# Kernel tuning notes

Measured on AMD Instinct MI355X. Metric: run time of the kernel, lower is better.

Reference implementation:

```python
import jax, jax.numpy as jnp
import numpy as np
from jax import lax

DIM = 384
HEADS = 8
CROP = 8


def conv2d(x, w, groups=1, pad=0):
    return lax.conv_general_dilated(
        x, w, (1, 1), ((pad, pad), (pad, pad)),
        dimension_numbers=("NCHW", "OIHW", "NCHW"),
        feature_group_count=groups)


def l2norm(x, axis):
    # F.normalize: x / max(||x||_2, 1e-12)
    n = jnp.sqrt(jnp.sum(x * x, axis=axis, keepdims=True))
    return x / jnp.maximum(n, 1e-12)


def masked_softmax(a, k):
    # top-k mask via k-th largest threshold (equivalent to scatter mask for
    # continuous-valued scores), then softmax with -inf fill.
    kth = lax.top_k(a, k)[0][..., -1:]
    return jax.nn.softmax(jnp.where(a >= kth, a, -jnp.inf), axis=-1)


def setup_inputs() -> dict:
    key = jax.random.key(0)
    ks = jax.random.split(key, 5)
    b, c, h, w = 2, DIM, 128, 128
    x = jax.random.normal(ks[0], (b, c, h, w), dtype=jnp.float32)
    w_qkv = jax.random.normal(ks[1], (3 * c, c, 1, 1), dtype=jnp.float32) * 0.02
    w_dw = jax.random.normal(ks[2], (3 * c, 1, 3, 3), dtype=jnp.float32) * 0.02
    w_proj = jax.random.normal(ks[3], (c, c, 1, 1), dtype=jnp.float32) * 0.02
    temperature = jnp.ones((HEADS, 1, 1), dtype=jnp.float32)
    a = jnp.full((1,), 0.2, dtype=jnp.float32)
    return {"x": x, "w_qkv": w_qkv, "w_dw": w_dw, "w_proj": w_proj,
            "temperature": temperature, "attn1": a, "attn2": a,
            "attn3": a, "attn4": a}


def reference(x, w_qkv, w_dw, w_proj, temperature, attn1, attn2, attn3, attn4):
    b, c, h, w = x.shape
    heads, crop = HEADS, CROP
    ch = c // heads                      # per-head channels C
    N = crop * crop                      # window tokens

    qkv = conv2d(conv2d(x, w_qkv), w_dw, groups=3 * c, pad=1)
    q, k, v = jnp.split(qkv, 3, axis=1)

    def to_heads(t):                     # b (head c) h w -> b head c (h w)
        return t.reshape(b, heads, ch, h * w)

    def to_win(t):                       # imgtowindows on (b, head, c, h, w)
        t = t.reshape(b, heads, ch, h // crop, crop, w // crop, crop)
        t = jnp.transpose(t, (0, 1, 3, 5, 4, 6, 2))
        return t.reshape(-1, heads, N, ch)

    qc, kc, vc = to_heads(q), to_heads(k), to_heads(v)
    qs = to_win(q.reshape(b, heads, ch, h, w))
    ks_ = to_win(k.reshape(b, heads, ch, h, w))
    vs = to_win(v.reshape(b, heads, ch, h, w))

    qc, kc = l2norm(qc, -1), l2norm(kc, -1)
    qs, ks_ = l2norm(qs, -1), l2norm(ks_, -1)

    cattn = jnp.einsum("bhcn,bhdn->bhcd", qc, kc) * temperature  # (b,H,C,C)
    sattn = jnp.einsum("bhnc,bhmc->bhnm", qs, ks_) * temperature  # (B',H,N,N)

    cks = [ch // 2, (ch * 2) // 3, (ch * 3) // 4, (ch * 4) // 5]
    sks = [N // 2, (N * 2) // 3, (N * 3) // 4, (N * 4) // 5]
    wts = [attn1, attn2, attn3, attn4]

    cout = sum((masked_softmax(cattn, kk) @ vc) * wt for kk, wt in zip(cks, wts))
    sout = sum((masked_softmax(sattn, kk) @ vs) * wt for kk, wt in zip(sks, wts))

    # windowstoimg (replicates torch's contiguous view/reshape semantics)
    sout = sout.reshape(b, heads, h, w, ch)
    sout = jnp.transpose(sout, (0, 1, 4, 2, 3)).reshape(b, heads, ch, h * w)

    out = (sout + cout).reshape(b, c, h, w)
    return conv2d(out, w_proj)
```

## Files before the change

kernel.cpp:

```cpp
#include <hip/hip_runtime.h>
#include <hip/hip_bf16.h>


#define HW 16384
#define CDIM 384
#define NHEADS 8
#define CH 48
#define NCHUNK 128

typedef __hip_bfloat16 bf16;
typedef __attribute__((ext_vector_type(8))) short short8;
typedef __attribute__((ext_vector_type(4))) float f32x4;

static __device__ __forceinline__ unsigned short f2bf_bits(float v) {
  bf16 b = __float2bfloat16(v);
  return __builtin_bit_cast(unsigned short, b);
}
static __device__ __forceinline__ float bfbits2f(unsigned short u) {
  return __bfloat162float(__builtin_bit_cast(bf16, u));
}

template <int CTRL>
static __device__ __forceinline__ float dppf(float x) {
  return __builtin_bit_cast(
      float, __builtin_amdgcn_update_dpp(0, __builtin_bit_cast(int, x), CTRL,
                                         0xF, 0xF, true));
}

__global__ __launch_bounds__(256) void decomp_all(const float* __restrict__ wq,
                                                  const float* __restrict__ wp,
                                                  unsigned short* __restrict__ qh,
                                                  unsigned short* __restrict__ ql,
                                                  unsigned short* __restrict__ ph,
                                                  unsigned short* __restrict__ pl) {
  const int i = blockIdx.x * 256 + threadIdx.x;
  const int nq = 3 * CDIM * CDIM;
  if (i < nq) {
    const float v = wq[i];
    const unsigned short hb = f2bf_bits(v);
    qh[i] = hb;
    ql[i] = f2bf_bits(v - bfbits2f(hb));
  } else {
    const int k = i - nq;
    if (k < CDIM * CDIM) {
      const float v = wp[k];
      const unsigned short hb = f2bf_bits(v);
      ph[k] = hb;
      pl[k] = f2bf_bits(v - bfbits2f(hb));
    }
  }
}

__global__ __launch_bounds__(256) void transpose_frag(const float* __restrict__ src,
                                                      short8* __restrict__ dh,
                                                      short8* __restrict__ dl,
                                                      float* __restrict__ sumsq) {
  if (blockIdx.x == 0 && threadIdx.x < 192) {
    const float4 z = {0.f, 0.f, 0.f, 0.f};
    ((float4*)sumsq)[threadIdx.x] = z;
  }
  const int o = blockIdx.x * 256 + threadIdx.x;
  const int ptile = o / 768;
  const int rem = o - ptile * 768;
  const int kc = rem >> 6, lane = rem & 63;
  const int p = ptile * 16 + (lane & 15);
  const int kb = kc * 32 + (lane >> 4) * 8;
  short8 hh, ll;
#pragma unroll
  for (int j = 0; j < 8; j++) {
    float v = src[(size_t)(kb + j) * HW + p];
    unsigned short hb = f2bf_bits(v);
    hh[j] = (short)hb;
    ll[j] = (short)f2bf_bits(v - bfbits2f(hb));
  }
  dh[o] = hh;
  dl[o] = ll;
}

__global__ __launch_bounds__(256, 4) void gemm_mfma(const unsigned short* __restrict__ Wh,
                                                    const unsigned short* __restrict__ Wl,
                                                    const short8* __restrict__ Xh,
                                                    const short8* __restrict__ Xl,
                                                    float* __restrict__ Out) {
  const int tid = threadIdx.x;
  const int wave = tid >> 6, lane = tid & 63;
  const int lm = lane & 15, lq = lane >> 4;
  const int g = blockIdx.y * 128 + blockIdx.x;
  const int xcd = g & 7, i = g >> 3;
  const int bx = xcd * 16 + (i & 15);
  const int by = i >> 4;
  const int p0 = bx * 128;
  const int oc0 = by * 64;
  const int pt0 = bx * 8 + wave * 2;
  f32x4 acc[4][2] = {};
#pragma unroll
  for (int kc = 0; kc < 12; kc++) {
    short8 ah[4], al[4], bh[2], bl[2];
#pragma unroll
    for (int mt = 0; mt < 4; mt++) {
      const size_t off = (size_t)(oc0 + mt * 16 + lm) * 384 + kc * 32 + lq * 8;
      ah[mt] = *reinterpret_cast<const short8*>(Wh + off);
      al[mt] = *reinterpret_cast<const short8*>(Wl + off);
    }
#pragma unroll
    for (int nt = 0; nt < 2; nt++) {
      const size_t idx = (size_t)((pt0 + nt) * 12 + kc) * 64 + lane;
      bh[nt] = Xh[idx];
      bl[nt] = Xl[idx];
    }
#pragma unroll
    for (int mt = 0; mt < 4; mt++)
#pragma unroll
      for (int nt = 0; nt < 2; nt++) {
        acc[mt][nt] = __builtin_amdgcn_mfma_f32_16x16x32_bf16(ah[mt], bh[nt], acc[mt][nt], 0, 0, 0);
        acc[mt][nt] = __builtin_amdgcn_mfma_f32_16x16x32_bf16(ah[mt], bl[nt], acc[mt][nt], 0, 0, 0);
        acc[mt][nt] = __builtin_amdgcn_mfma_f32_16x16x32_bf16(al[mt], bh[nt], acc[mt][nt], 0, 0, 0);
      }
  }
#pragma unroll
  for (int mt = 0; mt < 4; mt++)
#pragma unroll
    for (int nt = 0; nt < 2; nt++)
#pragma unroll
      for (int r = 0; r < 4; r++) {
        const int oc = oc0 + mt * 16 + lq * 4 + r;
        const int p = p0 + (wave * 2 + nt) * 16 + lm;
        Out[(size_t)oc * HW + p] = acc[mt][nt][r];
      }
}

__global__ __launch_bounds__(256) void dwconv3(const float* __restrict__ A,
                                               const float* __restrict__ wdw,
                                               float* __restrict__ Bq) {
  const int e = blockIdx.x * 256 + threadIdx.x;
  const int x4 = e & 31;
  const int y = (e >> 5) & 127;
  const int ch = e >> 12;
  const int x0 = x4 << 2;
  float w[9];
#pragma unroll
  for (int t = 0; t < 9; t++) w[t] = wdw[ch * 9 + t];
  const float* Ap = A + (size_t)ch * HW;
  float4 acc = {0.f, 0.f, 0.f, 0.f};
#pragma unroll
  for (int ky = 0; ky < 3; ky++) {
    const int yy = y + ky - 1;
    if (yy < 0 || yy > 127) continue;
    const float* row = Ap + yy * 128;
    const float4 c = *(const float4*)(row + x0);
    const float l = (x4 == 0) ? 0.f : row[x0 - 1];
    const float r = (x4 == 31) ? 0.f : row[x0 + 4];
    const float w0 = w[ky * 3], w1 = w[ky * 3 + 1], w2 = w[ky * 3 + 2];
    acc.x += w0 * l + w1 * c.x + w2 * c.y;
    acc.y += w0 * c.x + w1 * c.y + w2 * c.z;
    acc.z += w0 * c.y + w1 * c.z + w2 * c.w;
    acc.w += w0 * c.z + w1 * c.w + w2 * r;
  }
  *(float4*)(Bq + (size_t)e * 4) = acc;
}

__global__ __launch_bounds__(256, 3) void cattn_partial(const float* __restrict__ Bq,
                                                        float* __restrict__ part,
                                                        float* __restrict__ sumsq) {
  __shared__ __align__(16) float qs[48 * 132];
  __shared__ __align__(16) float ks2[48 * 132];
  const int tid = threadIdx.x;
  const int chunk = blockIdx.x, h = blockIdx.y;
  const int p0 = chunk * 128;
#pragma unroll
  for (int i = 0; i < 12; i++) {
    const int s4 = tid + i * 256;
    const int t = s4 >= 1536;
    const int r4 = s4 - t * 1536;
    const int cc = r4 >> 5;
    const int px = (r4 & 31) << 2;
    const float4 v4 = *(const float4*)(Bq + (size_t)(t * CDIM + h * CH + cc) * HW + p0 + px);
    *(float4*)((t ? ks2 : qs) + cc * 132 + px) = v4;
  }
  __syncthreads();
  if (tid < 96) {
    const int t = tid >= 48;
    const int cc = t ? tid - 48 : tid;
    const float* src = (t ? ks2 : qs) + cc * 132;
    float s = 0.f;
#pragma unroll
    for (int p = 0; p < 128; p += 4) {
      const float4 v = *(const float4*)(src + p);
      s += v.x * v.x + v.y * v.y + v.z * v.z + v.w * v.w;
    }
    atomicAdd(&sumsq[t * CDIM + h * CH + cc], s);
  }
  const int tx = tid & 15, ty = tid >> 4;
  const float* qb = qs + (ty * 3) * 132;
  const float* kb = ks2 + (tx * 3) * 132;
  float acc[3][3] = {};
  for (int pl = 0; pl < 128; pl += 4) {
    float4 qv[3], kv[3];
#pragma unroll
    for (int ii = 0; ii < 3; ii++) qv[ii] = *(const float4*)(qb + ii * 132 + pl);
#pragma unroll
    for (int jj = 0; jj < 3; jj++) kv[jj] = *(const float4*)(kb + jj * 132 + pl);
#pragma unroll
    for (int ii = 0; ii < 3; ii++)
#pragma unroll
      for (int jj = 0; jj < 3; jj++)
        acc[ii][jj] += qv[ii].x * kv[jj].x + qv[ii].y * kv[jj].y +
                       qv[ii].z * kv[jj].z + qv[ii].w * kv[jj].w;
  }
  float* rp = part + (size_t)(h * NCHUNK + chunk) * 2304;
#pragma unroll
  for (int ii = 0; ii < 3; ii++)
#pragma unroll
    for (int jj = 0; jj < 3; jj++)
      rp[(ty * 3 + ii) * 48 + tx * 3 + jj] = acc[ii][jj];
}

__global__ __launch_bounds__(64) void chan_softmax(
    const float* __restrict__ part, const float* __restrict__ sumsq,
    const float* __restrict__ temp, const float* __restrict__ a1,
    const float* __restrict__ a2, const float* __restrict__ a3,
    const float* __restrict__ a4, float* __restrict__ W48) {
  const int blk = blockIdx.x;
  const int i = blk % 48;
  const int h = blk / 48;
  const int lane = threadIdx.x;
  const float t = temp[h];
  float a = -3.0e38f;
  if (lane < 48) {
    const float* pp = part + (size_t)h * NCHUNK * 2304 + i * 48 + lane;
    float r = 0.f;
#pragma unroll 8
    for (int c = 0; c < NCHUNK; c++) r += pp[(size_t)c * 2304];
    const float iq = 1.f / fmaxf(sqrtf(sumsq[h * CH + i]), 1e-12f);
    const float ik = 1.f / fmaxf(sqrtf(sumsq[CDIM + h * CH + lane]), 1e-12f);
    a = t * iq * ik * r;
  }
  float m = a;
  for (int o = 32; o; o >>= 1) m = fmaxf(m, __shfl_xor(m, o));
  float e = (lane < 48) ? expf(a - m) : 0.f;
  int gt = 0;
  for (int j = 0; j < 48; j++) {
    float vj = __shfl(a, j);
    gt += (vj > a) ? 1 : 0;
  }
  const int ksel[4] = {24, 32, 36, 38};
  const float wts[4] = {a1[0], a2[0], a3[0], a4[0]};
  float coef = 0.f;
#pragma unroll
  for (int kk = 0; kk < 4; kk++) {
    float sel = (gt < ksel[kk]) ? e : 0.f;
    for (int o = 32; o; o >>= 1) sel += __shfl_xor(sel, o);
    if (gt < ksel[kk]) coef += wts[kk] / sel;
  }
  if (lane < 48) W48[(size_t)blk * 48 + lane] = e * coef;
}

static __device__ __forceinline__ void conv_frag_k(int f, const float* kRaw,
                                                   short8* KFh, short8* KFl) {
  int nt, ks, slot;
  if (f < 256) { nt = f >> 6; ks = 0; slot = f & 63; }
  else { const int g2 = f - 256; nt = g2 >> 5; ks = 1; slot = g2 & 31; }
  const int tok = nt * 16 + (slot & 15);
  const int ch0 = ks * 32 + (slot >> 4) * 8;
  const float* src = kRaw + tok * 49 + ch0;
  short8 hh, ll;
#pragma unroll
  for (int j = 0; j < 8; j++) {
    const float v = src[j];
    const unsigned short hb = f2bf_bits(v);
    hh[j] = (short)hb;
    ll[j] = (short)f2bf_bits(v - bfbits2f(hb));
  }
  KFh[f] = hh;
  KFl[f] = ll;
}
static __device__ __forceinline__ int wfrag_off(int f) {
  int nt, n, k0;
  if (f < 192) { nt = f >> 6; const int slot = f & 63; n = slot & 15; k0 = (slot >> 4) * 8; }
  else { const int g2 = f - 192; nt = g2 >> 5; const int slot = g2 & 31; n = slot & 15; k0 = 32 + (slot >> 4) * 8; }
  return (nt * 16 + n) * 48 + k0;
}

__global__ __launch_bounds__(256, 4) void spatial_kernel(
    const float* __restrict__ Bq, const float* __restrict__ W48,
    const float* __restrict__ temp, const float* __restrict__ a1,
    const float* __restrict__ a2_, const float* __restrict__ a3,
    const float* __restrict__ a4, float* __restrict__ Cbuf) {
  __shared__ __align__(16) char smem[40192];
  float* qRaw = (float*)smem;
  float* kRaw = (float*)(smem + 12544);
  short8* KFh = (short8*)(smem + 25088);
  short8* KFl = (short8*)(smem + 31232);
  float* S_lds = (float*)smem;
  unsigned short* VTh = (unsigned short*)(smem + 16640);
  unsigned short* VTl = (unsigned short*)(smem + 23552);
  bf16* Pl = (bf16*)(smem + 30464);
  short8* WFh = (short8*)smem;
  short8* WFl = (short8*)(smem + 4608);
  float* O_lds = (float*)(smem + 16640);
  float* invQ = (float*)(smem + 39680);
  float* invK = (float*)(smem + 39936);

  const int bid = blockIdx.x;
  const int wid = ((bid & 7) << 8) | (bid >> 3);
  const int wx = wid & 15, wy = (wid >> 4) & 15;
  const int head = wid >> 8;
  const int tid = threadIdx.x;
  const int lane = tid & 63, w = tid >> 6;
  const int lm = lane & 15, lq = lane >> 4;
  const int ybase = wy * 8, xbase = wx * 8;
  const int y_out = wy * 8 + (wx >> 1);
  const int x0 = (wx & 1) * 64;
  const size_t hb = (size_t)(head * CH) * HW;
  const float* wsrc = W48 + (size_t)head * 2304;

#pragma unroll
  for (int i = 0; i < 6; i++) {
    const int s4 = tid + i * 256;
    const int t = s4 >= 768;
    const int r4 = s4 - t * 768;
    const int cc = r4 >> 4, nq = r4 & 15;
    const int n = nq * 4;
    const int y = ybase + (n >> 3), x = xbase + (n & 7);
    const float4 v4 = *(const float4*)(Bq + (size_t)(t * CDIM) * HW + hb +
                                       (size_t)cc * HW + y * 128 + x);
    float* dst = (t ? kRaw : qRaw) + n * 49 + cc;
    dst[0] = v4.x; dst[49] = v4.y; dst[98] = v4.z; dst[147] = v4.w;
  }
  float wpre0[8], wpre1[8];
  {
    const int off = wfrag_off(tid);
    const float4 a = *(const float4*)(wsrc + off);
    const float4 b = *(const float4*)(wsrc + off + 4);
    wpre0[0] = a.x; wpre0[1] = a.y; wpre0[2] = a.z; wpre0[3] = a.w;
    wpre0[4] = b.x; wpre0[5] = b.y; wpre0[6] = b.z; wpre0[7] = b.w;
  }
  if (tid < 32) {
    const int off = wfrag_off(256 + tid);
    const float4 a = *(const float4*)(wsrc + off);
    const float4 b = *(const float4*)(wsrc + off + 4);
    wpre1[0] = a.x; wpre1[1] = a.y; wpre1[2] = a.z; wpre1[3] = a.w;
    wpre1[4] = b.x; wpre1[5] = b.y; wpre1[6] = b.z; wpre1[7] = b.w;
  }
  __syncthreads();

  float4 vv[3];
#pragma unroll
  for (int i = 0; i < 3; i++) {
    const int e4 = tid + i * 256;
    const int cc = e4 >> 4, n = (e4 & 15) * 4;
    const int y = ybase + (n >> 3), x = xbase + (n & 7);
    vv[i] = *(const float4*)(Bq + (size_t)(2 * CDIM) * HW + hb +
                             (size_t)cc * HW + y * 128 + x);
  }
  float af[16];
  {
    const int px = y_out * 128 + x0 + (w * 16 + lm);
    const float* vpl = Bq + (size_t)(2 * CDIM) * HW + hb + px;
#pragma unroll
    for (int ks = 0; ks < 2; ks++)
#pragma unroll
      for (int j = 0; j < 8; j++) {
        const int ch = ks * 32 + lq * 8 + j;
        af[ks * 8 + j] = (ch < 48) ? vpl[(size_t)ch * HW] : 0.f;
      }
  }

  if (tid < 128) {
    const int t = tid >> 6, n = tid & 63;
    const float* src = (t ? kRaw : qRaw) + n * 49;
    float ssum = 0.f;
#pragma unroll
    for (int cc = 0; cc < 48; cc++) { float v = src[cc]; ssum += v * v; }
    const float iv = 1.f / fmaxf(sqrtf(ssum), 1e-12f);
    if (t) invK[n] = iv; else invQ[n] = iv * temp[head];
  }

  conv_frag_k(tid, kRaw, KFh, KFl);
  if (tid < 128) conv_frag_k(256 + tid, kRaw, KFh, KFl);

  short8 qh[2], ql[2];
#pragma unroll
  for (int ks = 0; ks < 2; ks++) {
    const int ch0 = ks * 32 + lq * 8;
    const float* qp = qRaw + (w * 16 + lm) * 49 + ch0;
#pragma unroll
    for (int j = 0; j < 8; j++) {
      const float v = (ch0 < 48) ? qp[j] : 0.f;
      const unsigned short hbts = f2bf_bits(v);
      qh[ks][j] = (short)hbts;
      ql[ks][j] = (short)f2bf_bits(v - bfbits2f(hbts));
    }
  }
  __syncthreads();

  f32x4 sacc[4] = {};
#pragma unroll
  for (int nt = 0; nt < 4; nt++) {
    const short8 kh0 = KFh[nt * 64 + lane];
    const short8 kl0 = KFl[nt * 64 + lane];
    sacc[nt] = __builtin_amdgcn_mfma_f32_16x16x32_bf16(qh[0], kh0, sacc[nt], 0, 0, 0);
    sacc[nt] = __builtin_amdgcn_mfma_f32_16x16x32_bf16(qh[0], kl0, sacc[nt], 0, 0, 0);
    sacc[nt] = __builtin_amdgcn_mfma_f32_16x16x32_bf16(ql[0], kh0, sacc[nt], 0, 0, 0);
    short8 kh1 = {0, 0, 0, 0, 0, 0, 0, 0}, kl1 = {0, 0, 0, 0, 0, 0, 0, 0};
    if (lane < 32) { kh1 = KFh[256 + nt * 32 + lane]; kl1 = KFl[256 + nt * 32 + lane]; }
    sacc[nt] = __builtin_amdgcn_mfma_f32_16x16x32_bf16(qh[1], kh1, sacc[nt], 0, 0, 0);
    sacc[nt] = __builtin_amdgcn_mfma_f32_16x16x32_bf16(qh[1], kl1, sacc[nt], 0, 0, 0);
    sacc[nt] = __builtin_amdgcn_mfma_f32_16x16x32_bf16(ql[1], kh1, sacc[nt], 0, 0, 0);
  }

  float iqv[4];
#pragma unroll
  for (int r = 0; r < 4; r++) iqv[r] = invQ[w * 16 + lq * 4 + r];
#pragma unroll
  for (int nt = 0; nt < 4; nt++) {
    const float ik = invK[nt * 16 + lm];
#pragma unroll
    for (int r = 0; r < 4; r++)
      S_lds[(w * 16 + lq * 4 + r) * 65 + nt * 16 + lm] = sacc[nt][r] * iqv[r] * ik;
  }
  __syncthreads();

#pragma unroll
  for (int i = 0; i < 3; i++) {
    const int e4 = tid + i * 256;
    const int cc = e4 >> 4, n = (e4 & 15) * 4;
    const float v0 = vv[i].x, v1 = vv[i].y, v2 = vv[i].z, v3 = vv[i].w;
    const unsigned short h0 = f2bf_bits(v0), h1 = f2bf_bits(v1),
                         h2 = f2bf_bits(v2), h3 = f2bf_bits(v3);
    const ushort4 hh = {h0, h1, h2, h3};
    const ushort4 ll = {f2bf_bits(v0 - bfbits2f(h0)), f2bf_bits(v1 - bfbits2f(h1)),
                        f2bf_bits(v2 - bfbits2f(h2)), f2bf_bits(v3 - bfbits2f(h3))};
    *(ushort4*)(VTh + cc * 72 + n) = hh;
    *(ushort4*)(VTl + cc * 72 + n) = ll;
  }

  const float wts[4] = {a1[0], a2_[0], a3[0], a4[0]};
  const int sidx[4] = {32, 22, 16, 13};
#pragma unroll 4
  for (int rr = 0; rr < 16; rr++) {
    const int row = w * 16 + rr;
    const float a = S_lds[row * 65 + lane];
    float s = a;
#pragma unroll
    for (int k2 = 2; k2 <= 64; k2 <<= 1) {
#pragma unroll
      for (int j = k2 >> 1; j > 0; j >>= 1) {
        float o;
        if (j == 1)      o = dppf<0xB1>(s);
        else if (j == 2) o = dppf<0x4E>(s);
        else if (j == 8) o = dppf<0x128>(s);
        else             o = __shfl_xor(s, j);
        const bool up = ((lane & k2) == 0);
        const bool lower = ((lane & j) == 0);
        const float mn = fminf(s, o), mx = fmaxf(s, o);
        s = (lower == up) ? mn : mx;
      }
    }
    const float m = __shfl(s, 63);
    float v = __expf(s - m);
    v += dppf<0x101>(v);
    v += dppf<0x102>(v);
    v += dppf<0x104>(v);
    v += dppf<0x108>(v);
    const float t1 = __shfl(v, 16), t2 = __shfl(v, 32), t3 = __shfl(v, 48);
    const float beyond =
        (lq == 0) ? (t1 + t2 + t3) : (lq == 1) ? (t2 + t3) : (lq == 2) ? t3 : 0.f;
    const float suf = v + beyond;
    const float e = __expf(a - m);
    float coef = 0.f;
#pragma unroll
    for (int kk = 0; kk < 4; kk++) {
      const float tk = __shfl(s, sidx[kk]);
      const float Sk = __shfl(suf, sidx[kk]);
      if (a >= tk) coef += wts[kk] * __builtin_amdgcn_rcpf(Sk);
    }
    Pl[row * 72 + lane] = __float2bfloat16(e * coef);
  }
  __syncthreads();

  {
    short8 hh, ll;
#pragma unroll
    for (int j = 0; j < 8; j++) {
      const float v = wpre0[j];
      const unsigned short hbw = f2bf_bits(v);
      hh[j] = (short)hbw;
      ll[j] = (short)f2bf_bits(v - bfbits2f(hbw));
    }
    WFh[tid] = hh;
    WFl[tid] = ll;
  }
  if (tid < 32) {
    short8 hh, ll;
#pragma unroll
    for (int j = 0; j < 8; j++) {
      const float v = wpre1[j];
      const unsigned short hbw = f2bf_bits(v);
      hh[j] = (short)hbw;
      ll[j] = (short)f2bf_bits(v - bfbits2f(hbw));
    }
    WFh[256 + tid] = hh;
    WFl[256 + tid] = ll;
  }
  short8 pa[2];
#pragma unroll
  for (int ks = 0; ks < 2; ks++)
    pa[ks] = *reinterpret_cast<const short8*>(&Pl[(w * 16 + lm) * 72 + ks * 32 + lq * 8]);
  short8 a2h[2], a2l[2];
#pragma unroll
  for (int ks = 0; ks < 2; ks++)
#pragma unroll
    for (int j = 0; j < 8; j++) {
      const float v = af[ks * 8 + j];
      const unsigned short hv = f2bf_bits(v);
      a2h[ks][j] = (short)hv;
      a2l[ks][j] = (short)f2bf_bits(v - bfbits2f(hv));
    }
  __syncthreads();

  f32x4 oacc[3] = {};
#pragma unroll
  for (int nt = 0; nt < 3; nt++) {
    const int chv = nt * 16 + lm;
#pragma unroll
    for (int ks = 0; ks < 2; ks++) {
      const short8 vh = *reinterpret_cast<const short8*>(VTh + chv * 72 + ks * 32 + lq * 8);
      const short8 vl = *reinterpret_cast<const short8*>(VTl + chv * 72 + ks * 32 + lq * 8);
      oacc[nt] = __builtin_amdgcn_mfma_f32_16x16x32_bf16(pa[ks], vh, oacc[nt], 0, 0, 0);
      oacc[nt] = __builtin_amdgcn_mfma_f32_16x16x32_bf16(pa[ks], vl, oacc[nt], 0, 0, 0);
    }
    {
      const short8 wh0 = WFh[nt * 64 + lane];
      const short8 wl0 = WFl[nt * 64 + lane];
      oacc[nt] = __builtin_amdgcn_mfma_f32_16x16x32_bf16(a2h[0], wh0, oacc[nt], 0, 0, 0);
      oacc[nt] = __builtin_amdgcn_mfma_f32_16x16x32_bf16(a2h[0], wl0, oacc[nt], 0, 0, 0);
      oacc[nt] = __builtin_amdgcn_mfma_f32_16x16x32_bf16(a2l[0], wh0, oacc[nt], 0, 0, 0);
      short8 wh1 = {0, 0, 0, 0, 0, 0, 0, 0}, wl1 = {0, 0, 0, 0, 0, 0, 0, 0};
      if (lane < 32) { wh1 = WFh[192 + nt * 32 + lane]; wl1 = WFl[192 + nt * 32 + lane]; }
      oacc[nt] = __builtin_amdgcn_mfma_f32_16x16x32_bf16(a2h[1], wh1, oacc[nt], 0, 0, 0);
      oacc[nt] = __builtin_amdgcn_mfma_f32_16x16x32_bf16(a2h[1], wl1, oacc[nt], 0, 0, 0);
      oacc[nt] = __builtin_amdgcn_mfma_f32_16x16x32_bf16(a2l[1], wh1, oacc[nt], 0, 0, 0);
    }
  }
  __syncthreads();

#pragma unroll
  for (int nt = 0; nt < 3; nt++)
#pragma unroll
    for (int r = 0; r < 4; r++)
      O_lds[(nt * 16 + lm) * 65 + w * 16 + lq * 4 + r] = oacc[nt][r];
  __syncthreads();

#pragma unroll
  for (int i = 0; i < 3; i++) {
    const int s4 = tid + i * 256;
    const int cc = s4 >> 4, n = (s4 & 15) * 4;
    const float* op = O_lds + cc * 65 + n;
    const float4 o4 = {op[0], op[1], op[2], op[3]};
    *(float4*)(Cbuf + ((size_t)(head * CH + cc) * 128 + y_out) * 128 + x0 + n) = o4;
  }
}

extern "C" void kernel_launch(void* const* d_in, const int* in_sizes, int n_in,
                              void* d_out, int out_size, void* d_ws, size_t ws_size,
                              hipStream_t stream) {
  const float* x = (const float*)d_in[0];
  const float* w_qkv = (const float*)d_in[1];
  const float* w_dw = (const float*)d_in[2];
  const float* w_proj = (const float*)d_in[3];
  const float* temp = (const float*)d_in[4];
  const float* a1 = (const float*)d_in[5];
  const float* a2 = (const float*)d_in[6];
  const float* a3 = (const float*)d_in[7];
  const float* a4 = (const float*)d_in[8];
  float* out = (float*)d_out;

  char* ws = (char*)d_ws;
  float* cattn_part = (float*)ws;
  float* W48 = (float*)(ws + 9437184);
  float* sumsq = (float*)(ws + 9510912);
  unsigned short* wqkv_h = (unsigned short*)(ws + 9513984);
  unsigned short* wqkv_l = (unsigned short*)(ws + 10398720);
  unsigned short* wproj_h = (unsigned short*)(ws + 11283456);
  unsigned short* wproj_l = (unsigned short*)(ws + 11578368);
  float* Bq = (float*)(ws + 11873280);
  short8* Xtgh = (short8*)(ws + 11873280 + (size_t)2 * CDIM * HW * 4);
  short8* Xtgl = (short8*)(ws + 11873280 + (size_t)2 * CDIM * HW * 4 + 12582912);
  short8* Ctgh = (short8*)(ws + 11873280);
  short8* Ctgl = (short8*)(ws + 11873280 + 12582912);

  decomp_all<<<(4 * CDIM * CDIM + 255) / 256, 256, 0, stream>>>(
      w_qkv, w_proj, wqkv_h, wqkv_l, wproj_h, wproj_l);

  for (int b = 0; b < 2; b++) {
    const float* xb = x + (size_t)b * CDIM * HW;
    float* ob = out + (size_t)b * CDIM * HW;

    transpose_frag<<<3072, 256, 0, stream>>>(xb, Xtgh, Xtgl, sumsq);
    for (int t = 0; t < 3; t++) {
      gemm_mfma<<<dim3(HW / 128, CDIM / 64), 256, 0, stream>>>(
          wqkv_h + (size_t)t * CDIM * CDIM, wqkv_l + (size_t)t * CDIM * CDIM,
          Xtgh, Xtgl, ob);
      dwconv3<<<(CDIM * HW / 4) / 256, 256, 0, stream>>>(
          ob, w_dw + (size_t)t * CDIM * 9, Bq + (size_t)t * CDIM * HW);
    }

    cattn_partial<<<dim3(NCHUNK, NHEADS), 256, 0, stream>>>(Bq, cattn_part, sumsq);
    chan_softmax<<<NHEADS * 48, 64, 0, stream>>>(cattn_part, sumsq, temp, a1, a2, a3, a4, W48);
    spatial_kernel<<<NHEADS * 256, 256, 0, stream>>>(Bq, W48, temp, a1, a2, a3, a4, ob);

    transpose_frag<<<3072, 256, 0, stream>>>(ob, Ctgh, Ctgl, sumsq);
    gemm_mfma<<<dim3(HW / 128, CDIM / 64), 256, 0, stream>>>(wproj_h, wproj_l,
                                                             Ctgh, Ctgl, ob);
  }

  (void)in_sizes; (void)n_in; (void)out_size; (void)ws_size;
}
```

Before: 735.1 us.

## Shrink spatial kernel LDS footprint via aliasing and register-shuffled scores

New measurement: 736.3 us. About the same (+0.2%).

```diff
diff --git a/kernel.cpp b/kernel.cpp
--- a/kernel.cpp
+++ b/kernel.cpp
@@ -255,25 +255,6 @@
   if (lane < 48) W48[(size_t)blk * 48 + lane] = e * coef;
 }
 
-static __device__ __forceinline__ void conv_frag_k(int f, const float* kRaw,
-                                                   short8* KFh, short8* KFl) {
-  int nt, ks, slot;
-  if (f < 256) { nt = f >> 6; ks = 0; slot = f & 63; }
-  else { const int g2 = f - 256; nt = g2 >> 5; ks = 1; slot = g2 & 31; }
-  const int tok = nt * 16 + (slot & 15);
-  const int ch0 = ks * 32 + (slot >> 4) * 8;
-  const float* src = kRaw + tok * 49 + ch0;
-  short8 hh, ll;
-#pragma unroll
-  for (int j = 0; j < 8; j++) {
-    const float v = src[j];
-    const unsigned short hb = f2bf_bits(v);
-    hh[j] = (short)hb;
-    ll[j] = (short)f2bf_bits(v - bfbits2f(hb));
-  }
-  KFh[f] = hh;
-  KFl[f] = ll;
-}
 static __device__ __forceinline__ int wfrag_off(int f) {
   int nt, n, k0;
   if (f < 192) { nt = f >> 6; const int slot = f & 63; n = slot & 15; k0 = (slot >> 4) * 8; }
@@ -281,25 +262,24 @@
   return (nt * 16 + n) * 48 + k0;
 }
 
-__global__ __launch_bounds__(256, 4) void spatial_kernel(
+__global__ __launch_bounds__(256, 5) void spatial_kernel(
     const float* __restrict__ Bq, const float* __restrict__ W48,
     const float* __restrict__ temp, const float* __restrict__ a1,
     const float* __restrict__ a2_, const float* __restrict__ a3,
     const float* __restrict__ a4, float* __restrict__ Cbuf) {
-  __shared__ __align__(16) char smem[40192];
+  __shared__ __align__(16) char smem[25600];
   float* qRaw = (float*)smem;
   float* kRaw = (float*)(smem + 12544);
-  short8* KFh = (short8*)(smem + 25088);
-  short8* KFl = (short8*)(smem + 31232);
-  float* S_lds = (float*)smem;
-  unsigned short* VTh = (unsigned short*)(smem + 16640);
-  unsigned short* VTl = (unsigned short*)(smem + 23552);
-  bf16* Pl = (bf16*)(smem + 30464);
-  short8* WFh = (short8*)smem;
-  short8* WFl = (short8*)(smem + 4608);
-  float* O_lds = (float*)(smem + 16640);
-  float* invQ = (float*)(smem + 39680);
-  float* invK = (float*)(smem + 39936);
+  short8* KFh = (short8*)smem;
+  short8* KFl = (short8*)(smem + 6144);
+  bf16* Pl = (bf16*)(smem + 12544);
+  unsigned short* VTh = (unsigned short*)smem;
+  unsigned short* VTl = (unsigned short*)(smem + 7680);
+  short8* WFh = (short8*)(smem + 15360);
+  short8* WFl = (short8*)(smem + 19968);
+  float* O_lds = (float*)smem;
+  float* invQ = (float*)(smem + 25088);
+  float* invK = (float*)(smem + 25344);
 
   const int bid = blockIdx.x;
   const int wid = ((bid & 7) << 8) | (bid >> 3);
@@ -327,21 +307,6 @@
     float* dst = (t ? kRaw : qRaw) + n * 49 + cc;
     dst[0] = v4.x; dst[49] = v4.y; dst[98] = v4.z; dst[147] = v4.w;
   }
-  float wpre0[8], wpre1[8];
-  {
-    const int off = wfrag_off(tid);
-    const float4 a = *(const float4*)(wsrc + off);
-    const float4 b = *(const float4*)(wsrc + off + 4);
-    wpre0[0] = a.x; wpre0[1] = a.y; wpre0[2] = a.z; wpre0[3] = a.w;
-    wpre0[4] = b.x; wpre0[5] = b.y; wpre0[6] = b.z; wpre0[7] = b.w;
-  }
-  if (tid < 32) {
-    const int off = wfrag_off(256 + tid);
-    const float4 a = *(const float4*)(wsrc + off);
-    const float4 b = *(const float4*)(wsrc + off + 4);
-    wpre1[0] = a.x; wpre1[1] = a.y; wpre1[2] = a.z; wpre1[3] = a.w;
-    wpre1[4] = b.x; wpre1[5] = b.y; wpre1[6] = b.z; wpre1[7] = b.w;
-  }
   __syncthreads();
 
   float4 vv[3];
@@ -376,8 +341,29 @@
     if (t) invK[n] = iv; else invQ[n] = iv * temp[head];
   }
 
-  conv_frag_k(tid, kRaw, KFh, KFl);
-  if (tid < 128) conv_frag_k(256 + tid, kRaw, KFh, KFl);
+  short8 kh0r, kl0r, kh1r, kl1r;
+  {
+    const int nt = tid >> 6, slot = tid & 63;
+    const float* src = kRaw + (nt * 16 + (slot & 15)) * 49 + (slot >> 4) * 8;
+#pragma unroll
+    for (int j = 0; j < 8; j++) {
+      const float v = src[j];
+      const unsigned short hbk = f2bf_bits(v);
+      kh0r[j] = (short)hbk;
+      kl0r[j] = (short)f2bf_bits(v - bfbits2f(hbk));
+    }
+  }
+  if (tid < 128) {
+    const int nt = tid >> 5, slot = tid & 31;
+    const float* src = kRaw + (nt * 16 + (slot & 15)) * 49 + 32 + (slot >> 4) * 8;
+#pragma unroll
+    for (int j = 0; j < 8; j++) {
+      const float v = src[j];
+      const unsigned short hbk = f2bf_bits(v);
+      kh1r[j] = (short)hbk;
+      kl1r[j] = (short)f2bf_bits(v - bfbits2f(hbk));
+    }
+  }
 
   short8 qh[2], ql[2];
 #pragma unroll
@@ -392,6 +378,11 @@
       ql[ks][j] = (short)f2bf_bits(v - bfbits2f(hbts));
     }
   }
+  __syncthreads();
+
+  KFh[tid] = kh0r;
+  KFl[tid] = kl0r;
+  if (tid < 128) { KFh[256 + tid] = kh1r; KFl[256 + tid] = kl1r; }
   __syncthreads();
 
   f32x4 sacc[4] = {};
@@ -409,38 +400,19 @@
     sacc[nt] = __builtin_amdgcn_mfma_f32_16x16x32_bf16(ql[1], kh1, sacc[nt], 0, 0, 0);
   }
 
-  float iqv[4];
-#pragma unroll
-  for (int r = 0; r < 4; r++) iqv[r] = invQ[w * 16 + lq * 4 + r];
-#pragma unroll
-  for (int nt = 0; nt < 4; nt++) {
-    const float ik = invK[nt * 16 + lm];
-#pragma unroll
-    for (int r = 0; r < 4; r++)
-      S_lds[(w * 16 + lq * 4 + r) * 65 + nt * 16 + lm] = sacc[nt][r] * iqv[r] * ik;
-  }
-  __syncthreads();
-
-#pragma unroll
-  for (int i = 0; i < 3; i++) {
-    const int e4 = tid + i * 256;
-    const int cc = e4 >> 4, n = (e4 & 15) * 4;
-    const float v0 = vv[i].x, v1 = vv[i].y, v2 = vv[i].z, v3 = vv[i].w;
-    const unsigned short h0 = f2bf_bits(v0), h1 = f2bf_bits(v1),
-                         h2 = f2bf_bits(v2), h3 = f2bf_bits(v3);
-    const ushort4 hh = {h0, h1, h2, h3};
-    const ushort4 ll = {f2bf_bits(v0 - bfbits2f(h0)), f2bf_bits(v1 - bfbits2f(h1)),
-                        f2bf_bits(v2 - bfbits2f(h2)), f2bf_bits(v3 - bfbits2f(h3))};
-    *(ushort4*)(VTh + cc * 72 + n) = hh;
-    *(ushort4*)(VTl + cc * 72 + n) = ll;
-  }
-
   const float wts[4] = {a1[0], a2_[0], a3[0], a4[0]};
   const int sidx[4] = {32, 22, 16, 13};
-#pragma unroll 4
+  const float ikl = invK[lane];
+#pragma unroll
   for (int rr = 0; rr < 16; rr++) {
-    const int row = w * 16 + rr;
-    const float a = S_lds[row * 65 + lane];
+    const int lqR = rr >> 2, rR = rr & 3;
+    const int srcl = lqR * 16 + lm;
+    const float t0 = __shfl(sacc[0][rR], srcl);
+    const float t1 = __shfl(sacc[1][rR], srcl);
+    const float t2 = __shfl(sacc[2][rR], srcl);
+    const float t3 = __shfl(sacc[3][rR], srcl);
+    const float araw = (lq == 0) ? t0 : (lq == 1) ? t1 : (lq == 2) ? t2 : t3;
+    const float a = araw * invQ[w * 16 + rr] * ikl;
     float s = a;
 #pragma unroll
     for (int k2 = 2; k2 <= 64; k2 <<= 1) {
@@ -463,9 +435,9 @@
     v += dppf<0x102>(v);
     v += dppf<0x104>(v);
     v += dppf<0x108>(v);
-    const float t1 = __shfl(v, 16), t2 = __shfl(v, 32), t3 = __shfl(v, 48);
+    const float t1s = __shfl(v, 16), t2s = __shfl(v, 32), t3s = __shfl(v, 48);
     const float beyond =
-        (lq == 0) ? (t1 + t2 + t3) : (lq == 1) ? (t2 + t3) : (lq == 2) ? t3 : 0.f;
+        (lq == 0) ? (t1s + t2s + t3s) : (lq == 1) ? (t2s + t3s) : (lq == 2) ? t3s : 0.f;
     const float suf = v + beyond;
     const float e = __expf(a - m);
     float coef = 0.f;
@@ -475,38 +447,57 @@
       const float Sk = __shfl(suf, sidx[kk]);
       if (a >= tk) coef += wts[kk] * __builtin_amdgcn_rcpf(Sk);
     }
-    Pl[row * 72 + lane] = __float2bfloat16(e * coef);
-  }
-  __syncthreads();
-
+    Pl[(w * 16 + rr) * 80 + lane] = __float2bfloat16(e * coef);
+  }
+  short8 pa[2];
+#pragma unroll
+  for (int ks = 0; ks < 2; ks++)
+    pa[ks] = *reinterpret_cast<const short8*>(&Pl[(w * 16 + lm) * 80 + ks * 32 + lq * 8]);
+  __syncthreads();
+
+#pragma unroll
+  for (int i = 0; i < 3; i++) {
+    const int e4 = tid + i * 256;
+    const int cc = e4 >> 4, n = (e4 & 15) * 4;
+    const float v0 = vv[i].x, v1 = vv[i].y, v2 = vv[i].z, v3 = vv[i].w;
+    const unsigned short h0 = f2bf_bits(v0), h1 = f2bf_bits(v1),
+                         h2 = f2bf_bits(v2), h3 = f2bf_bits(v3);
+    const ushort4 hh = {h0, h1, h2, h3};
+    const ushort4 ll = {f2bf_bits(v0 - bfbits2f(h0)), f2bf_bits(v1 - bfbits2f(h1)),
+                        f2bf_bits(v2 - bfbits2f(h2)), f2bf_bits(v3 - bfbits2f(h3))};
+    *(ushort4*)(VTh + cc * 80 + n) = hh;
+    *(ushort4*)(VTl + cc * 80 + n) = ll;
+  }
   {
+    const int off = wfrag_off(tid);
+    const float4 aw = *(const float4*)(wsrc + off);
+    const float4 bw = *(const float4*)(wsrc + off + 4);
+    const float wv[8] = {aw.x, aw.y, aw.z, aw.w, bw.x, bw.y, bw.z, bw.w};
     short8 hh, ll;
 #pragma unroll
     for (int j = 0; j < 8; j++) {
-      const float v = wpre0[j];
-      const unsigned short hbw = f2bf_bits(v);
+      const unsigned short hbw = f2bf_bits(wv[j]);
       hh[j] = (short)hbw;
-      ll[j] = (short)f2bf_bits(v - bfbits2f(hbw));
+      ll[j] = (short)f2bf_bits(wv[j] - bfbits2f(hbw));
     }
     WFh[tid] = hh;
     WFl[tid] = ll;
   }
   if (tid < 32) {
+    const int off = wfrag_off(256 + tid);
+    const float4 aw = *(const float4*)(wsrc + off);
+    const float4 bw = *(const float4*)(wsrc + off + 4);
+    const float wv[8] = {aw.x, aw.y, aw.z, aw.w, bw.x, bw.y, bw.z, bw.w};
     short8 hh, ll;
 #pragma unroll
     for (int j = 0; j < 8; j++) {
-      const float v = wpre1[j];
-      const unsigned short hbw = f2bf_bits(v);
+      const unsigned short hbw = f2bf_bits(wv[j]);
       hh[j] = (short)hbw;
-      ll[j] = (short)f2bf_bits(v - bfbits2f(hbw));
+      ll[j] = (short)f2bf_bits(wv[j] - bfbits2f(hbw));
     }
     WFh[256 + tid] = hh;
     WFl[256 + tid] = ll;
   }
-  short8 pa[2];
-#pragma unroll
-  for (int ks = 0; ks < 2; ks++)
-    pa[ks] = *reinterpret_cast<const short8*>(&Pl[(w * 16 + lm) * 72 + ks * 32 + lq * 8]);
   short8 a2h[2], a2l[2];
 #pragma unroll
   for (int ks = 0; ks < 2; ks++)
@@ -525,8 +516,8 @@
     const int chv = nt * 16 + lm;
 #pragma unroll
     for (int ks = 0; ks < 2; ks++) {
-      const short8 vh = *reinterpret_cast<const short8*>(VTh + chv * 72 + ks * 32 + lq * 8);
-      const short8 vl = *reinterpret_cast<const short8*>(VTl + chv * 72 + ks * 32 + lq * 8);
+      const short8 vh = *reinterpret_cast<const short8*>(VTh + chv * 80 + ks * 32 + lq * 8);
+      const short8 vl = *reinterpret_cast<const short8*>(VTl + chv * 80 + ks * 32 + lq * 8);
       oacc[nt] = __builtin_amdgcn_mfma_f32_16x16x32_bf16(pa[ks], vh, oacc[nt], 0, 0, 0);
       oacc[nt] = __builtin_amdgcn_mfma_f32_16x16x32_bf16(pa[ks], vl, oacc[nt], 0, 0, 0);
     }
```
